# Kernel optimization log

Hardware: AMD Instinct MI355X
Metric: run time of the kernel (lower is better)

## Reference

```python
import jax, jax.numpy as jnp
import numpy as np

N = 50000
E = 800000
IN_CH = 128
HID = 128
HEADS = 8
OUT_CH = 40
NEG_SLOPE = 0.2
BN_EPS = 1e-5


def gat_conv(x, src, dst, W, a_src, a_dst, bias, heads, ch, concat):
    # x: [N, F_in]; W: [heads*ch, F_in]; a_src/a_dst: [heads, ch]; bias: [heads*ch] or [ch]
    n = x.shape[0]
    h = (x @ W.T).reshape(n, heads, ch)                      # [N, H, C]
    alpha_src = (h * a_src[None]).sum(-1)                    # [N, H]
    alpha_dst = (h * a_dst[None]).sum(-1)                    # [N, H]
    e = alpha_src[src] + alpha_dst[dst]                      # [E, H]
    e = jax.nn.leaky_relu(e, NEG_SLOPE)
    # segment softmax over incoming edges of each destination node
    emax = jax.ops.segment_max(e, dst, num_segments=n)       # [N, H]
    ee = jnp.exp(e - emax[dst])
    denom = jax.ops.segment_sum(ee, dst, num_segments=n)     # [N, H]
    alpha = ee / (denom[dst] + 1e-16)                        # [E, H]
    msg = h[src] * alpha[:, :, None]                         # [E, H, C]
    out = jax.ops.segment_sum(msg, dst, num_segments=n)      # [N, H, C]
    out = out.reshape(n, heads * ch) if concat else out.mean(axis=1)
    return out + bias


def batch_norm_eval(x, gamma, beta, mean, var):
    return (x - mean) * jax.lax.rsqrt(var + BN_EPS) * gamma + beta


def setup_inputs() -> dict:
    key = jax.random.key(0)
    ks = jax.random.split(key, 16)
    ch = HID // HEADS  # 16
    s = 1.0 / np.sqrt(IN_CH)
    inp = {
        "x": jax.random.normal(ks[0], (N, IN_CH), dtype=jnp.float32),
        "edge_index": jax.random.randint(ks[1], (2, E), 0, N, dtype=jnp.int64),
        # layer 0
        "W0": jax.random.normal(ks[2], (HEADS * ch, IN_CH), jnp.float32) * s,
        "a_src0": jax.random.normal(ks[3], (HEADS, ch), jnp.float32) * 0.1,
        "a_dst0": jax.random.normal(ks[4], (HEADS, ch), jnp.float32) * 0.1,
        "b0": jnp.zeros((HID,), jnp.float32),
        "bn_g0": jnp.ones((HID,), jnp.float32),
        "bn_b0": jnp.zeros((HID,), jnp.float32),
        "bn_m0": jnp.zeros((HID,), jnp.float32),
        "bn_v0": jnp.ones((HID,), jnp.float32),
        # layer 1
        "W1": jax.random.normal(ks[5], (HEADS * ch, HID), jnp.float32) * (1.0 / np.sqrt(HID)),
        "a_src1": jax.random.normal(ks[6], (HEADS, ch), jnp.float32) * 0.1,
        "a_dst1": jax.random.normal(ks[7], (HEADS, ch), jnp.float32) * 0.1,
        "b1": jnp.zeros((HID,), jnp.float32),
        "bn_g1": jnp.ones((HID,), jnp.float32),
        "bn_b1": jnp.zeros((HID,), jnp.float32),
        "bn_m1": jnp.zeros((HID,), jnp.float32),
        "bn_v1": jnp.ones((HID,), jnp.float32),
        # output layer (heads=1, concat=False)
        "W2": jax.random.normal(ks[8], (OUT_CH, HID), jnp.float32) * (1.0 / np.sqrt(HID)),
        "a_src2": jax.random.normal(ks[9], (1, OUT_CH), jnp.float32) * 0.1,
        "a_dst2": jax.random.normal(ks[10], (1, OUT_CH), jnp.float32) * 0.1,
        "b2": jnp.zeros((OUT_CH,), jnp.float32),
    }
    return inp


def reference(x, edge_index, W0, a_src0, a_dst0, b0, bn_g0, bn_b0, bn_m0, bn_v0,
              W1, a_src1, a_dst1, b1, bn_g1, bn_b1, bn_m1, bn_v1,
              W2, a_src2, a_dst2, b2):
    n = x.shape[0]
    # PyG GATConv adds self-loops by default
    loops = jnp.arange(n, dtype=edge_index.dtype)
    src = jnp.concatenate([edge_index[0], loops])
    dst = jnp.concatenate([edge_index[1], loops])
    ch = HID // HEADS

    h = gat_conv(x, src, dst, W0, a_src0, a_dst0, b0, HEADS, ch, True)
    h = batch_norm_eval(h, bn_g0, bn_b0, bn_m0, bn_v0)
    h = jax.nn.elu(h)
    # dropout: eval mode (identity)

    h = gat_conv(h, src, dst, W1, a_src1, a_dst1, b1, HEADS, ch, True)
    h = batch_norm_eval(h, bn_g1, bn_b1, bn_m1, bn_v1)
    h = jax.nn.elu(h)

    out = gat_conv(h, src, dst, W2, a_src2, a_dst2, b2, 1, OUT_CH, False)
    return out
```

## Files before the change

### kernel.cpp

```cpp
#include <hip/hip_runtime.h>
#include <hip/hip_fp16.h>
#include <math.h>

constexpr float NEG_SLOPE = 0.2f;
constexpr float BN_EPS_C = 1e-5f;

using half8 = __attribute__((ext_vector_type(8))) _Float16;
using half4 = __attribute__((ext_vector_type(4))) _Float16;
using f32x4 = __attribute__((ext_vector_type(4))) float;


__global__ __launch_bounds__(256)
void hist_cvt_kernel(const int* __restrict__ ei, int* __restrict__ bucket_count,
                     int E, int N, int NEB,
                     const float* __restrict__ W0, const float* __restrict__ W1,
                     const float* __restrict__ W2,
                     __half* __restrict__ W0h, __half* __restrict__ W1h,
                     __half* __restrict__ W2h) {
    int t = threadIdx.x;
    if ((int)blockIdx.x >= NEB) {
        int i = ((int)blockIdx.x - NEB) * 256 + t;
        if (i < 16384) {
            W0h[i] = __float2half(W0[i]);
            W1h[i] = __float2half(W1[i]);
        }
        if (i < 6144) W2h[i] = __float2half(i < 5120 ? W2[i] : 0.f);
        return;
    }
    __shared__ int h[256];
    h[t] = 0;
    __syncthreads();
    int base = blockIdx.x * 8192;
    int ET = E + N;
#pragma unroll
    for (int q = 0; q < 32; ++q) {
        int i = base + q * 256 + t;
        if (i < ET) {
            int d = (i < E) ? ei[E + i] : (i - E);
            atomicAdd(&h[d >> 8], 1);
        }
    }
    __syncthreads();
    if (h[t] > 0) atomicAdd(&bucket_count[t], h[t]);
}

__global__ __launch_bounds__(256)
void bucket_scan_kernel(const int* __restrict__ bucket_count, int* __restrict__ bucket_ptr,
                        int* __restrict__ gcursor, int* __restrict__ row_ptr,
                        int N, int ET) {
    __shared__ int s[256];
    int t = threadIdx.x;
    int c = bucket_count[t];
    s[t] = c;
    __syncthreads();
    for (int off = 1; off < 256; off <<= 1) {
        int v = (t >= off) ? s[t - off] : 0;
        __syncthreads();
        s[t] += v;
        __syncthreads();
    }
    int excl = s[t] - c;
    bucket_ptr[t] = excl;
    gcursor[t] = excl;
    if (t == 255) {
        bucket_ptr[256] = s[255];
        row_ptr[N] = ET;
    }
}

__global__ __launch_bounds__(256)
void bucket_bin_kernel(const int* __restrict__ ei, int* __restrict__ gcursor,
                       unsigned* __restrict__ tmp, int E, int N) {
    __shared__ unsigned bins[8192];
    __shared__ int lcount[256];
    __shared__ int lofs[256];
    __shared__ int lbase[256];
    __shared__ int lcur[256];
    int t = threadIdx.x;
    lcount[t] = 0;
    __syncthreads();
    int base = blockIdx.x * 8192;
    int ET = E + N;
    unsigned pr[32];
#pragma unroll
    for (int q = 0; q < 32; ++q) {
        int i = base + q * 256 + t;
        pr[q] = 0xFFFFFFFFu;
        if (i < ET) {
            int s, d;
            if (i < E) { s = ei[i]; d = ei[E + i]; }
            else       { s = i - E; d = s; }
            pr[q] = ((unsigned)d << 16) | (unsigned)s;
            atomicAdd(&lcount[d >> 8], 1);
        }
    }
    __syncthreads();
    {
        int c = lcount[t];
        lofs[t] = c;
        __syncthreads();
        for (int off = 1; off < 256; off <<= 1) {
            int v = (t >= off) ? lofs[t - off] : 0;
            __syncthreads();
            lofs[t] += v;
            __syncthreads();
        }
        int excl = lofs[t] - c;
        __syncthreads();
        lofs[t] = excl;
        lcur[t] = excl;
        if (c > 0) lbase[t] = atomicAdd(&gcursor[t], c);
    }
    __syncthreads();
#pragma unroll
    for (int q = 0; q < 32; ++q) {
        if (pr[q] != 0xFFFFFFFFu) {
            int b = pr[q] >> 24;
            int p = atomicAdd(&lcur[b], 1);
            bins[p] = pr[q];
        }
    }
    __syncthreads();
    int total = min(8192, ET - base);
    for (int p = t; p < total; p += 256) {
        unsigned e = bins[p];
        int b = e >> 24;
        tmp[lbase[b] + (p - lofs[b])] = e;
    }
}

__global__ __launch_bounds__(256)
void fine_scatter_kernel(const unsigned* __restrict__ tmp, const int* __restrict__ bucket_ptr,
                         int* __restrict__ row_ptr, int* __restrict__ srcs, int N) {
    __shared__ int hist[256];
    __shared__ int scanb[256];
    __shared__ int cur[256];
    int b = blockIdx.x, t = threadIdx.x;
    int base = bucket_ptr[b];
    int cnt = bucket_ptr[b + 1] - base;
    int n0 = b << 8;
    hist[t] = 0;
    __syncthreads();
    for (int p = t; p < cnt; p += 256)
        atomicAdd(&hist[(int)(tmp[base + p] >> 16) - n0], 1);
    __syncthreads();
    int c = hist[t];
    scanb[t] = c;
    __syncthreads();
    for (int off = 1; off < 256; off <<= 1) {
        int v = (t >= off) ? scanb[t - off] : 0;
        __syncthreads();
        scanb[t] += v;
        __syncthreads();
    }
    int excl = scanb[t] - c;
    cur[t] = excl;
    if (n0 + t < N) row_ptr[n0 + t] = base + excl;
    __syncthreads();
    for (int p = t; p < cnt; p += 256) {
        unsigned e = tmp[base + p];
        int pos = atomicAdd(&cur[(int)(e >> 16) - n0], 1);
        srcs[base + pos] = (int)(e & 0xFFFFu);
    }
}


template<bool AHALF>
__global__ __launch_bounds__(512)
void gemm128_mfma_kernel(const void* __restrict__ Xv, const __half* __restrict__ W16,
                         const float* __restrict__ a_src, const float* __restrict__ a_dst,
                         __half* __restrict__ hp, float* __restrict__ asrc,
                         float* __restrict__ adst, int N) {
    __shared__ _Float16 Bs[128][136];
    const int t = threadIdx.x;
    const int n0 = blockIdx.x * 128;

#pragma unroll
    for (int i = 0; i < 4; ++i) {
        int lin = t + i * 512;
        int n = lin >> 4;
        int m = lin & 15;
        *reinterpret_cast<uint4*>(&Bs[n][8 * m]) =
            *reinterpret_cast<const uint4*>(&W16[(size_t)n * 128 + 8 * m]);
    }
    __syncthreads();

    const int l  = t & 63;
    const int w  = t >> 6;
    const int lr = l & 15;
    const int lg = l >> 4;
    const int rowA = n0 + 16 * w + lr;
    const bool rokA = rowA < N;

    f32x4 acc[8];
#pragma unroll
    for (int tt = 0; tt < 8; ++tt) acc[tt] = (f32x4){0.f, 0.f, 0.f, 0.f};

#pragma unroll
    for (int ks = 0; ks < 4; ++ks) {
        half8 a;
        if (rokA) {
            if constexpr (AHALF) {
                const __half* X = (const __half*)Xv;
                a = *reinterpret_cast<const half8*>(&X[(size_t)rowA * 128 + 8 * lg + 32 * ks]);
            } else {
                const float* X = (const float*)Xv;
                const float* p = &X[(size_t)rowA * 128 + 8 * lg + 32 * ks];
                float4 v0 = *reinterpret_cast<const float4*>(p);
                float4 v1 = *reinterpret_cast<const float4*>(p + 4);
                a[0] = (_Float16)v0.x; a[1] = (_Float16)v0.y;
                a[2] = (_Float16)v0.z; a[3] = (_Float16)v0.w;
                a[4] = (_Float16)v1.x; a[5] = (_Float16)v1.y;
                a[6] = (_Float16)v1.z; a[7] = (_Float16)v1.w;
            }
        } else {
#pragma unroll
            for (int q = 0; q < 8; ++q) a[q] = (_Float16)0.f;
        }
#pragma unroll
        for (int tt = 0; tt < 8; ++tt) {
            half8 b = *reinterpret_cast<const half8*>(&Bs[16 * tt + lr][8 * lg + 32 * ks]);
            acc[tt] = __builtin_amdgcn_mfma_f32_16x16x32_f16(a, b, acc[tt], 0, 0, 0);
        }
    }

    float av[8], bv[8];
#pragma unroll
    for (int tt = 0; tt < 8; ++tt) {
        av[tt] = a_src[16 * tt + lr];
        bv[tt] = a_dst[16 * tt + lr];
    }
#pragma unroll
    for (int reg = 0; reg < 4; ++reg) {
        int gr = n0 + 16 * w + 4 * lg + reg;
        bool ok = gr < N;
        if (ok) {
#pragma unroll
            for (int tt = 0; tt < 8; ++tt)
                hp[(size_t)gr * 128 + 16 * tt + lr] = __float2half(acc[tt][reg]);
        }
#pragma unroll
        for (int tt = 0; tt < 8; ++tt) {
            float p = acc[tt][reg] * av[tt];
            float q = acc[tt][reg] * bv[tt];
#pragma unroll
            for (int off = 1; off < 16; off <<= 1) {
                p += __shfl_xor(p, off, 16);
                q += __shfl_xor(q, off, 16);
            }
            if (ok && lr == tt) {
                asrc[(size_t)gr * 8 + tt] = p;
                adst[(size_t)gr * 8 + tt] = q;
            }
        }
    }
}


__global__ __launch_bounds__(256)
void gemm40_mfma_kernel(const __half* __restrict__ X, const __half* __restrict__ W16,
                        const float* __restrict__ a_src, const float* __restrict__ a_dst,
                        __half* __restrict__ hp, float* __restrict__ asrc,
                        float* __restrict__ adst, int N) {
    __shared__ _Float16 Bs[48][136];
    const int t = threadIdx.x;
    const int n0 = blockIdx.x * 64;

#pragma unroll
    for (int i = 0; i < 3; ++i) {
        int lin = t + i * 256;
        if (lin < 768) {
            int n = lin >> 4;
            int m = lin & 15;
            *reinterpret_cast<uint4*>(&Bs[n][8 * m]) =
                *reinterpret_cast<const uint4*>(&W16[(size_t)n * 128 + 8 * m]);
        }
    }
    __syncthreads();

    const int l  = t & 63;
    const int w  = t >> 6;
    const int lr = l & 15;
    const int lg = l >> 4;
    const int rowA = n0 + 16 * w + lr;
    const bool rokA = rowA < N;

    f32x4 acc[3];
#pragma unroll
    for (int tt = 0; tt < 3; ++tt) acc[tt] = (f32x4){0.f, 0.f, 0.f, 0.f};

#pragma unroll
    for (int ks = 0; ks < 4; ++ks) {
        half8 a;
        if (rokA) {
            a = *reinterpret_cast<const half8*>(&X[(size_t)rowA * 128 + 8 * lg + 32 * ks]);
        } else {
#pragma unroll
            for (int q = 0; q < 8; ++q) a[q] = (_Float16)0.f;
        }
#pragma unroll
        for (int tt = 0; tt < 3; ++tt) {
            half8 b = *reinterpret_cast<const half8*>(&Bs[16 * tt + lr][8 * lg + 32 * ks]);
            acc[tt] = __builtin_amdgcn_mfma_f32_16x16x32_f16(a, b, acc[tt], 0, 0, 0);
        }
    }

    float av[3], bv[3];
#pragma unroll
    for (int tt = 0; tt < 3; ++tt) {
        int j = 16 * tt + lr;
        av[tt] = (j < 40) ? a_src[j] : 0.f;
        bv[tt] = (j < 40) ? a_dst[j] : 0.f;
    }
#pragma unroll
    for (int reg = 0; reg < 4; ++reg) {
        int gr = n0 + 16 * w + 4 * lg + reg;
        bool ok = gr < N;
        float p = 0.f, q = 0.f;
#pragma unroll
        for (int tt = 0; tt < 3; ++tt) {
            int j = 16 * tt + lr;
            if (ok && j < 40) hp[(size_t)gr * 40 + j] = __float2half(acc[tt][reg]);
            p += acc[tt][reg] * av[tt];
            q += acc[tt][reg] * bv[tt];
        }
#pragma unroll
        for (int off = 1; off < 16; off <<= 1) {
            p += __shfl_xor(p, off, 16);
            q += __shfl_xor(q, off, 16);
        }
        if (ok && lr == 0) {
            asrc[gr] = p;
            adst[gr] = q;
        }
    }
}


__global__ __launch_bounds__(256)
void message128_kernel(const __half* __restrict__ hh, const int* __restrict__ row_ptr,
                       const int* __restrict__ srcs,
                       const float* __restrict__ asrc, const float* __restrict__ adst,
                       const float* __restrict__ bias,
                       const float* __restrict__ bn_g, const float* __restrict__ bn_b,
                       const float* __restrict__ bn_m, const float* __restrict__ bn_v,
                       __half* __restrict__ out16, int N) {
    int node = blockIdx.x * 8 + (threadIdx.x >> 5);
    if (node >= N) return;
    int tc = threadIdx.x & 31;
    int half_id = tc >> 4;
    int cl = tc & 15;
    int hd = cl >> 1;
    int beg = row_ptr[node], end = row_ptr[node + 1];
    float ad = adst[(size_t)node * 8 + hd];
    float ssum = 0.f;
    float acc[8];
#pragma unroll
    for (int q = 0; q < 8; ++q) acc[q] = 0.f;

    int j = beg;
    for (; j + 4 <= end; j += 4) {
        int sA = srcs[j + half_id];
        int sB = srcs[j + 2 + half_id];
        half8 vA = *reinterpret_cast<const half8*>(&hh[(size_t)sA * 128 + 8 * cl]);
        half8 vB = *reinterpret_cast<const half8*>(&hh[(size_t)sB * 128 + 8 * cl]);
        float eA = asrc[(size_t)sA * 8 + hd] + ad;
        float eB = asrc[(size_t)sB * 8 + hd] + ad;
        eA = (eA > 0.f) ? eA : NEG_SLOPE * eA;
        eB = (eB > 0.f) ? eB : NEG_SLOPE * eB;
        float wA = __expf(eA);
        float wB = __expf(eB);
        ssum += wA + wB;
#pragma unroll
        for (int q = 0; q < 8; ++q) {
            acc[q] = fmaf((float)vA[q], wA, acc[q]);
            acc[q] = fmaf((float)vB[q], wB, acc[q]);
        }
    }
    for (; j + 2 <= end; j += 2) {
        int s = srcs[j + half_id];
        half8 v = *reinterpret_cast<const half8*>(&hh[(size_t)s * 128 + 8 * cl]);
        float e = asrc[(size_t)s * 8 + hd] + ad;
        e = (e > 0.f) ? e : NEG_SLOPE * e;
        float wgt = __expf(e);
        ssum += wgt;
#pragma unroll
        for (int q = 0; q < 8; ++q) acc[q] = fmaf((float)v[q], wgt, acc[q]);
    }
    if (j < end && half_id == 0) {
        int s = srcs[j];
        half8 v = *reinterpret_cast<const half8*>(&hh[(size_t)s * 128 + 8 * cl]);
        float e = asrc[(size_t)s * 8 + hd] + ad;
        e = (e > 0.f) ? e : NEG_SLOPE * e;
        float wgt = __expf(e);
        ssum += wgt;
#pragma unroll
        for (int q = 0; q < 8; ++q) acc[q] = fmaf((float)v[q], wgt, acc[q]);
    }
    ssum += __shfl_xor(ssum, 16);
#pragma unroll
    for (int q = 0; q < 8; ++q) acc[q] += __shfl_xor(acc[q], 16);

    if (half_id == 0) {
        float inv = 1.0f / (ssum + 1e-16f);
        int c = cl * 8;
        float r[8];
#pragma unroll
        for (int pp = 0; pp < 2; ++pp) {
            int cc = c + 4 * pp;
            float4 bi = *reinterpret_cast<const float4*>(&bias[cc]);
            float4 g  = *reinterpret_cast<const float4*>(&bn_g[cc]);
            float4 bb = *reinterpret_cast<const float4*>(&bn_b[cc]);
            float4 mm = *reinterpret_cast<const float4*>(&bn_m[cc]);
            float4 vv = *reinterpret_cast<const float4*>(&bn_v[cc]);
            r[4 * pp + 0] = (acc[4 * pp + 0] * inv + bi.x - mm.x) * rsqrtf(vv.x + BN_EPS_C) * g.x + bb.x;
            r[4 * pp + 1] = (acc[4 * pp + 1] * inv + bi.y - mm.y) * rsqrtf(vv.y + BN_EPS_C) * g.y + bb.y;
            r[4 * pp + 2] = (acc[4 * pp + 2] * inv + bi.z - mm.z) * rsqrtf(vv.z + BN_EPS_C) * g.z + bb.z;
            r[4 * pp + 3] = (acc[4 * pp + 3] * inv + bi.w - mm.w) * rsqrtf(vv.w + BN_EPS_C) * g.w + bb.w;
        }
        half8 o;
#pragma unroll
        for (int q = 0; q < 8; ++q) {
            float rv = (r[q] > 0.f) ? r[q] : expm1f(r[q]);
            o[q] = (_Float16)rv;
        }
        *reinterpret_cast<half8*>(&out16[(size_t)node * 128 + c]) = o;
    }
}


__global__ __launch_bounds__(256)
void message40_kernel(const __half* __restrict__ hh2, const int* __restrict__ row_ptr,
                      const int* __restrict__ srcs,
                      const float* __restrict__ asrc, const float* __restrict__ adst,
                      const float* __restrict__ b2, float* __restrict__ out, int N) {
    int node = blockIdx.x * 16 + (threadIdx.x >> 4);
    if (node >= N) return;
    int tc = threadIdx.x & 15;
    int beg = row_ptr[node], end = row_ptr[node + 1];
    float ad = adst[node];
    float ssum = 0.f;
    float acc[4] = {0.f, 0.f, 0.f, 0.f};
    int j = beg;
    for (; j + 2 <= end; j += 2) {
        int s0 = srcs[j];
        int s1 = srcs[j + 1];
        half4 v0 = (half4){0, 0, 0, 0}, v1 = (half4){0, 0, 0, 0};
        if (tc < 10) {
            v0 = *reinterpret_cast<const half4*>(&hh2[(size_t)s0 * 40 + 4 * tc]);
            v1 = *reinterpret_cast<const half4*>(&hh2[(size_t)s1 * 40 + 4 * tc]);
        }
        float e0 = asrc[s0] + ad;
        float e1 = asrc[s1] + ad;
        e0 = (e0 > 0.f) ? e0 : NEG_SLOPE * e0;
        e1 = (e1 > 0.f) ? e1 : NEG_SLOPE * e1;
        float w0 = __expf(e0);
        float w1 = __expf(e1);
        ssum += w0 + w1;
#pragma unroll
        for (int q = 0; q < 4; ++q) {
            acc[q] = fmaf((float)v0[q], w0, acc[q]);
            acc[q] = fmaf((float)v1[q], w1, acc[q]);
        }
    }
    if (j < end) {
        int s0 = srcs[j];
        half4 v0 = (half4){0, 0, 0, 0};
        if (tc < 10) v0 = *reinterpret_cast<const half4*>(&hh2[(size_t)s0 * 40 + 4 * tc]);
        float e0 = asrc[s0] + ad;
        e0 = (e0 > 0.f) ? e0 : NEG_SLOPE * e0;
        float w0 = __expf(e0);
        ssum += w0;
#pragma unroll
        for (int q = 0; q < 4; ++q) acc[q] = fmaf((float)v0[q], w0, acc[q]);
    }
    if (tc < 10) {
        float inv = 1.0f / (ssum + 1e-16f);
        int c = tc * 4;
        float4 bi = *reinterpret_cast<const float4*>(&b2[c]);
        *reinterpret_cast<float4*>(&out[(size_t)node * 40 + c]) =
            make_float4(acc[0] * inv + bi.x, acc[1] * inv + bi.y,
                        acc[2] * inv + bi.z, acc[3] * inv + bi.w);
    }
}


static inline char* align256(char* p) {
    return (char*)(((uintptr_t)p + 255) & ~(uintptr_t)255);
}

extern "C" void kernel_launch(void* const* d_in, const int* in_sizes, int n_in,
                              void* d_out, int out_size, void* d_ws, size_t ws_size,
                              hipStream_t stream) {
    const float* x   = (const float*)d_in[0];
    const int*   ei  = (const int*)d_in[1];
    const float* W0  = (const float*)d_in[2];
    const float* as0 = (const float*)d_in[3];
    const float* ad0 = (const float*)d_in[4];
    const float* b0  = (const float*)d_in[5];
    const float* g0  = (const float*)d_in[6];
    const float* bb0 = (const float*)d_in[7];
    const float* m0  = (const float*)d_in[8];
    const float* v0  = (const float*)d_in[9];
    const float* W1  = (const float*)d_in[10];
    const float* as1 = (const float*)d_in[11];
    const float* ad1 = (const float*)d_in[12];
    const float* b1  = (const float*)d_in[13];
    const float* g1  = (const float*)d_in[14];
    const float* bb1 = (const float*)d_in[15];
    const float* m1  = (const float*)d_in[16];
    const float* v1  = (const float*)d_in[17];
    const float* W2  = (const float*)d_in[18];
    const float* as2 = (const float*)d_in[19];
    const float* ad2 = (const float*)d_in[20];
    const float* b2  = (const float*)d_in[21];

    const int N  = in_sizes[0] / 128;
    const int E  = in_sizes[1] / 2;
    const int ET = E + N;
    const int NBUK = (N + 255) >> 8;
    const int NEB  = (ET + 8191) / 8192;

    char* wsp = (char*)d_ws;
    int* bucket_count = (int*)wsp;  wsp = align256(wsp + 256 * 4);
    int* bucket_ptr   = (int*)wsp;  wsp = align256(wsp + 257 * 4);
    int* gcursor      = (int*)wsp;  wsp = align256(wsp + 256 * 4);
    int* row_ptr      = (int*)wsp;  wsp = align256(wsp + (size_t)(N + 1) * 4);
    unsigned* tmp     = (unsigned*)wsp; wsp = align256(wsp + (size_t)ET * 4);
    int* srcs         = (int*)wsp;  wsp = align256(wsp + (size_t)ET * 4);
    __half* hh        = (__half*)wsp; wsp = align256(wsp + (size_t)N * 128 * 2);
    __half* h2        = (__half*)wsp; wsp = align256(wsp + (size_t)N * 40 * 2);
    __half* feat      = (__half*)wsp; wsp = align256(wsp + (size_t)N * 128 * 2);
    float* asr        = (float*)wsp;  wsp = align256(wsp + (size_t)N * 8 * 4);
    float* adt        = (float*)wsp;  wsp = align256(wsp + (size_t)N * 8 * 4);
    __half* W0h       = (__half*)wsp; wsp = align256(wsp + 16384 * 2);
    __half* W1h       = (__half*)wsp; wsp = align256(wsp + 16384 * 2);
    __half* W2h       = (__half*)wsp; wsp = align256(wsp + 6144 * 2);

    hipMemsetAsync(bucket_count, 0, 256 * 4, stream);
    hist_cvt_kernel<<<NEB + 64, 256, 0, stream>>>(ei, bucket_count, E, N, NEB,
                                                  W0, W1, W2, W0h, W1h, W2h);
    bucket_scan_kernel<<<1, 256, 0, stream>>>(bucket_count, bucket_ptr, gcursor, row_ptr, N, ET);
    bucket_bin_kernel<<<NEB, 256, 0, stream>>>(ei, gcursor, tmp, E, N);
    fine_scatter_kernel<<<NBUK, 256, 0, stream>>>(tmp, bucket_ptr, row_ptr, srcs, N);

    const int g128 = (N + 127) / 128;
    const int g64  = (N + 63) / 64;

    gemm128_mfma_kernel<false><<<g128, 512, 0, stream>>>(x, W0h, as0, ad0, hh, asr, adt, N);
    message128_kernel<<<(N + 7) / 8, 256, 0, stream>>>(hh, row_ptr, srcs, asr, adt,
                                                       b0, g0, bb0, m0, v0, feat, N);
    gemm128_mfma_kernel<true><<<g128, 512, 0, stream>>>(feat, W1h, as1, ad1, hh, asr, adt, N);
    message128_kernel<<<(N + 7) / 8, 256, 0, stream>>>(hh, row_ptr, srcs, asr, adt,
                                                       b1, g1, bb1, m1, v1, feat, N);
    gemm40_mfma_kernel<<<g64, 256, 0, stream>>>(feat, W2h, as2, ad2, h2, asr, adt, N);
    message40_kernel<<<(N + 15) / 16, 256, 0, stream>>>(h2, row_ptr, srcs,
                                                        asr, adt, b2, (float*)d_out, N);
}
```

Before: 213.4 us.

## Store hidden features head-sliced and split message passing per head slice

Hidden features and attention logits move from node-major to head-slice-major storage ([8][N][16] and [8][N]). The GEMMs write and read this layout, and the message kernel now gives each block one head slice for four nodes. A wavefront handles 16 edges at once with 4 lanes per edge and reduces across lanes with shuffles. The goal is to keep each slice's gather working set small enough for L2 and to parallelise over edges, at the cost of 8x more blocks and per-slice rereads of srcs and row_ptr.

```diff
diff --git a/kernel.cpp b/kernel.cpp
--- a/kernel.cpp
+++ b/kernel.cpp
@@ -202,7 +202,11 @@
         if (rokA) {
             if constexpr (AHALF) {
                 const __half* X = (const __half*)Xv;
-                a = *reinterpret_cast<const half8*>(&X[(size_t)rowA * 128 + 8 * lg + 32 * ks]);
+                int ch = 8 * lg + 32 * ks;
+                int sl = ch >> 4;
+                int off = ch & 15;
+                a = *reinterpret_cast<const half8*>(
+                    &X[(size_t)sl * N * 16 + (size_t)rowA * 16 + off]);
             } else {
                 const float* X = (const float*)Xv;
                 const float* p = &X[(size_t)rowA * 128 + 8 * lg + 32 * ks];
@@ -237,7 +241,7 @@
         if (ok) {
 #pragma unroll
             for (int tt = 0; tt < 8; ++tt)
-                hp[(size_t)gr * 128 + 16 * tt + lr] = __float2half(acc[tt][reg]);
+                hp[(size_t)tt * N * 16 + (size_t)gr * 16 + lr] = __float2half(acc[tt][reg]);
         }
 #pragma unroll
         for (int tt = 0; tt < 8; ++tt) {
@@ -249,8 +253,8 @@
                 q += __shfl_xor(q, off, 16);
             }
             if (ok && lr == tt) {
-                asrc[(size_t)gr * 8 + tt] = p;
-                adst[(size_t)gr * 8 + tt] = q;
+                asrc[(size_t)tt * N + gr] = p;
+                adst[(size_t)tt * N + gr] = q;
             }
         }
     }
@@ -293,7 +297,11 @@
     for (int ks = 0; ks < 4; ++ks) {
         half8 a;
         if (rokA) {
-            a = *reinterpret_cast<const half8*>(&X[(size_t)rowA * 128 + 8 * lg + 32 * ks]);
+            int ch = 8 * lg + 32 * ks;
+            int sl = ch >> 4;
+            int off = ch & 15;
+            a = *reinterpret_cast<const half8*>(
+                &X[(size_t)sl * N * 16 + (size_t)rowA * 16 + off]);
         } else {
 #pragma unroll
             for (int q = 0; q < 8; ++q) a[q] = (_Float16)0.f;
@@ -338,93 +346,68 @@
 
 
 __global__ __launch_bounds__(256)
-void message128_kernel(const __half* __restrict__ hh, const int* __restrict__ row_ptr,
+void message128_kernel(const __half* __restrict__ hhs, const int* __restrict__ row_ptr,
                        const int* __restrict__ srcs,
-                       const float* __restrict__ asrc, const float* __restrict__ adst,
+                       const float* __restrict__ asrc_s, const float* __restrict__ adst_s,
                        const float* __restrict__ bias,
                        const float* __restrict__ bn_g, const float* __restrict__ bn_b,
                        const float* __restrict__ bn_m, const float* __restrict__ bn_v,
-                       __half* __restrict__ out16, int N) {
-    int node = blockIdx.x * 8 + (threadIdx.x >> 5);
+                       __half* __restrict__ feat_s, int N) {
+    const int slice = blockIdx.x & 7;
+    const int node = (blockIdx.x >> 3) * 4 + (threadIdx.x >> 6);
     if (node >= N) return;
-    int tc = threadIdx.x & 31;
-    int half_id = tc >> 4;
-    int cl = tc & 15;
-    int hd = cl >> 1;
-    int beg = row_ptr[node], end = row_ptr[node + 1];
-    float ad = adst[(size_t)node * 8 + hd];
+    const int l = threadIdx.x & 63;
+    const int e = l >> 2;
+    const int q = l & 3;
+    const int beg = row_ptr[node], end = row_ptr[node + 1];
+    const __half* hsl = hhs + (size_t)slice * N * 16;
+    const float*  asl = asrc_s + (size_t)slice * N;
+    const float ad = adst_s[(size_t)slice * N + node];
+
     float ssum = 0.f;
-    float acc[8];
-#pragma unroll
-    for (int q = 0; q < 8; ++q) acc[q] = 0.f;
-
-    int j = beg;
-    for (; j + 4 <= end; j += 4) {
-        int sA = srcs[j + half_id];
-        int sB = srcs[j + 2 + half_id];
-        half8 vA = *reinterpret_cast<const half8*>(&hh[(size_t)sA * 128 + 8 * cl]);
-        half8 vB = *reinterpret_cast<const half8*>(&hh[(size_t)sB * 128 + 8 * cl]);
-        float eA = asrc[(size_t)sA * 8 + hd] + ad;
-        float eB = asrc[(size_t)sB * 8 + hd] + ad;
-        eA = (eA > 0.f) ? eA : NEG_SLOPE * eA;
-        eB = (eB > 0.f) ? eB : NEG_SLOPE * eB;
-        float wA = __expf(eA);
-        float wB = __expf(eB);
-        ssum += wA + wB;
-#pragma unroll
-        for (int q = 0; q < 8; ++q) {
-            acc[q] = fmaf((float)vA[q], wA, acc[q]);
-            acc[q] = fmaf((float)vB[q], wB, acc[q]);
-        }
-    }
-    for (; j + 2 <= end; j += 2) {
-        int s = srcs[j + half_id];
-        half8 v = *reinterpret_cast<const half8*>(&hh[(size_t)s * 128 + 8 * cl]);
-        float e = asrc[(size_t)s * 8 + hd] + ad;
-        e = (e > 0.f) ? e : NEG_SLOPE * e;
-        float wgt = __expf(e);
-        ssum += wgt;
-#pragma unroll
-        for (int q = 0; q < 8; ++q) acc[q] = fmaf((float)v[q], wgt, acc[q]);
-    }
-    if (j < end && half_id == 0) {
-        int s = srcs[j];
-        half8 v = *reinterpret_cast<const half8*>(&hh[(size_t)s * 128 + 8 * cl]);
-        float e = asrc[(size_t)s * 8 + hd] + ad;
-        e = (e > 0.f) ? e : NEG_SLOPE * e;
-        float wgt = __expf(e);
-        ssum += wgt;
-#pragma unroll
-        for (int q = 0; q < 8; ++q) acc[q] = fmaf((float)v[q], wgt, acc[q]);
-    }
-    ssum += __shfl_xor(ssum, 16);
-#pragma unroll
-    for (int q = 0; q < 8; ++q) acc[q] += __shfl_xor(acc[q], 16);
-
-    if (half_id == 0) {
+    float acc[4] = {0.f, 0.f, 0.f, 0.f};
+    for (int j = beg; j < end; j += 16) {
+        int idx = j + e;
+        float w = 0.f;
+        half4 v = (half4){0, 0, 0, 0};
+        if (idx < end) {
+            int s = srcs[idx];
+            v = *reinterpret_cast<const half4*>(&hsl[(size_t)s * 16 + 4 * q]);
+            float ea = asl[s] + ad;
+            ea = (ea > 0.f) ? ea : NEG_SLOPE * ea;
+            w = __expf(ea);
+        }
+        ssum += w;
+#pragma unroll
+        for (int k = 0; k < 4; ++k) acc[k] = fmaf((float)v[k], w, acc[k]);
+    }
+#pragma unroll
+    for (int off = 4; off < 64; off <<= 1) {
+        ssum += __shfl_xor(ssum, off);
+#pragma unroll
+        for (int k = 0; k < 4; ++k) acc[k] += __shfl_xor(acc[k], off);
+    }
+
+    if (e == 0) {
         float inv = 1.0f / (ssum + 1e-16f);
-        int c = cl * 8;
-        float r[8];
-#pragma unroll
-        for (int pp = 0; pp < 2; ++pp) {
-            int cc = c + 4 * pp;
-            float4 bi = *reinterpret_cast<const float4*>(&bias[cc]);
-            float4 g  = *reinterpret_cast<const float4*>(&bn_g[cc]);
-            float4 bb = *reinterpret_cast<const float4*>(&bn_b[cc]);
-            float4 mm = *reinterpret_cast<const float4*>(&bn_m[cc]);
-            float4 vv = *reinterpret_cast<const float4*>(&bn_v[cc]);
-            r[4 * pp + 0] = (acc[4 * pp + 0] * inv + bi.x - mm.x) * rsqrtf(vv.x + BN_EPS_C) * g.x + bb.x;
-            r[4 * pp + 1] = (acc[4 * pp + 1] * inv + bi.y - mm.y) * rsqrtf(vv.y + BN_EPS_C) * g.y + bb.y;
-            r[4 * pp + 2] = (acc[4 * pp + 2] * inv + bi.z - mm.z) * rsqrtf(vv.z + BN_EPS_C) * g.z + bb.z;
-            r[4 * pp + 3] = (acc[4 * pp + 3] * inv + bi.w - mm.w) * rsqrtf(vv.w + BN_EPS_C) * g.w + bb.w;
-        }
-        half8 o;
-#pragma unroll
-        for (int q = 0; q < 8; ++q) {
-            float rv = (r[q] > 0.f) ? r[q] : expm1f(r[q]);
-            o[q] = (_Float16)rv;
-        }
-        *reinterpret_cast<half8*>(&out16[(size_t)node * 128 + c]) = o;
+        int c = slice * 16 + 4 * q;
+        float4 bi = *reinterpret_cast<const float4*>(&bias[c]);
+        float4 g  = *reinterpret_cast<const float4*>(&bn_g[c]);
+        float4 bb = *reinterpret_cast<const float4*>(&bn_b[c]);
+        float4 mm = *reinterpret_cast<const float4*>(&bn_m[c]);
+        float4 vv = *reinterpret_cast<const float4*>(&bn_v[c]);
+        float r0 = (acc[0] * inv + bi.x - mm.x) * rsqrtf(vv.x + BN_EPS_C) * g.x + bb.x;
+        float r1 = (acc[1] * inv + bi.y - mm.y) * rsqrtf(vv.y + BN_EPS_C) * g.y + bb.y;
+        float r2 = (acc[2] * inv + bi.z - mm.z) * rsqrtf(vv.z + BN_EPS_C) * g.z + bb.z;
+        float r3 = (acc[3] * inv + bi.w - mm.w) * rsqrtf(vv.w + BN_EPS_C) * g.w + bb.w;
+        r0 = (r0 > 0.f) ? r0 : expm1f(r0);
+        r1 = (r1 > 0.f) ? r1 : expm1f(r1);
+        r2 = (r2 > 0.f) ? r2 : expm1f(r2);
+        r3 = (r3 > 0.f) ? r3 : expm1f(r3);
+        half4 o;
+        o[0] = (_Float16)r0; o[1] = (_Float16)r1;
+        o[2] = (_Float16)r2; o[3] = (_Float16)r3;
+        *reinterpret_cast<half4*>(&feat_s[(size_t)slice * N * 16 + (size_t)node * 16 + 4 * q]) = o;
     }
 }
 
@@ -546,13 +529,14 @@
 
     const int g128 = (N + 127) / 128;
     const int g64  = (N + 63) / 64;
+    const int gmsg = ((N + 3) / 4) * 8;
 
     gemm128_mfma_kernel<false><<<g128, 512, 0, stream>>>(x, W0h, as0, ad0, hh, asr, adt, N);
-    message128_kernel<<<(N + 7) / 8, 256, 0, stream>>>(hh, row_ptr, srcs, asr, adt,
-                                                       b0, g0, bb0, m0, v0, feat, N);
+    message128_kernel<<<gmsg, 256, 0, stream>>>(hh, row_ptr, srcs, asr, adt,
+                                                b0, g0, bb0, m0, v0, feat, N);
     gemm128_mfma_kernel<true><<<g128, 512, 0, stream>>>(feat, W1h, as1, ad1, hh, asr, adt, N);
-    message128_kernel<<<(N + 7) / 8, 256, 0, stream>>>(hh, row_ptr, srcs, asr, adt,
-                                                       b1, g1, bb1, m1, v1, feat, N);
+    message128_kernel<<<gmsg, 256, 0, stream>>>(hh, row_ptr, srcs, asr, adt,
+                                                b1, g1, bb1, m1, v1, feat, N);
     gemm40_mfma_kernel<<<g64, 256, 0, stream>>>(feat, W2h, as2, ad2, h2, asr, adt, N);
     message40_kernel<<<(N + 15) / 16, 256, 0, stream>>>(h2, row_ptr, srcs,
                                                         asr, adt, b2, (float*)d_out, N);
```

Result: slower. 425.5 us (+99.4%).

## Split GAT layers into edge-weight precompute and head-sliced aggregation

Applied to the files above, without the earlier changes.

Adds separate kernels that compute per-edge attention weights (stored as fp16, head-major) and per-node inverse softmax denominators. The 128-wide features move to a head-sliced layout ([8][N][16]), and the aggregation kernel now runs one block slice per head, so each gathered row fits in a small contiguous region. The aim is to take exp and leaky-relu work out of the gather loop and to improve cache locality per head slice. The cost is extra kernel launches, writing and reading an ET*8 fp16 weight array, fp16 rounding of the weights, and edge indices being re-read by every head slice.

```diff
diff --git a/kernel.cpp b/kernel.cpp
--- a/kernel.cpp
+++ b/kernel.cpp
@@ -202,7 +202,11 @@
         if (rokA) {
             if constexpr (AHALF) {
                 const __half* X = (const __half*)Xv;
-                a = *reinterpret_cast<const half8*>(&X[(size_t)rowA * 128 + 8 * lg + 32 * ks]);
+                int ch = 8 * lg + 32 * ks;
+                int sl = ch >> 4;
+                int off = ch & 15;
+                a = *reinterpret_cast<const half8*>(
+                    &X[(size_t)sl * N * 16 + (size_t)rowA * 16 + off]);
             } else {
                 const float* X = (const float*)Xv;
                 const float* p = &X[(size_t)rowA * 128 + 8 * lg + 32 * ks];
@@ -237,7 +241,7 @@
         if (ok) {
 #pragma unroll
             for (int tt = 0; tt < 8; ++tt)
-                hp[(size_t)gr * 128 + 16 * tt + lr] = __float2half(acc[tt][reg]);
+                hp[(size_t)tt * N * 16 + (size_t)gr * 16 + lr] = __float2half(acc[tt][reg]);
         }
 #pragma unroll
         for (int tt = 0; tt < 8; ++tt) {
@@ -293,7 +297,11 @@
     for (int ks = 0; ks < 4; ++ks) {
         half8 a;
         if (rokA) {
-            a = *reinterpret_cast<const half8*>(&X[(size_t)rowA * 128 + 8 * lg + 32 * ks]);
+            int ch = 8 * lg + 32 * ks;
+            int sl = ch >> 4;
+            int off = ch & 15;
+            a = *reinterpret_cast<const half8*>(
+                &X[(size_t)sl * N * 16 + (size_t)rowA * 16 + off]);
         } else {
 #pragma unroll
             for (int q = 0; q < 8; ++q) a[q] = (_Float16)0.f;
@@ -338,125 +346,138 @@
 
 
 __global__ __launch_bounds__(256)
-void message128_kernel(const __half* __restrict__ hh, const int* __restrict__ row_ptr,
+void weight8_kernel(const int* __restrict__ row_ptr, const int* __restrict__ srcs,
+                    const float* __restrict__ as8, const float* __restrict__ ad8,
+                    __half* __restrict__ ew, float* __restrict__ inv, int N, int ET) {
+    int gid = blockIdx.x * 256 + threadIdx.x;
+    int node = gid >> 3;
+    int h = gid & 7;
+    if (node >= N) return;
+    int beg = row_ptr[node], end = row_ptr[node + 1];
+    float ad = ad8[(size_t)node * 8 + h];
+    float sum = 0.f;
+    for (int j = beg; j < end; ++j) {
+        int s = srcs[j];
+        float e = as8[(size_t)s * 8 + h] + ad;
+        e = (e > 0.f) ? e : NEG_SLOPE * e;
+        float w = __expf(e);
+        sum += w;
+        ew[(size_t)h * ET + j] = __float2half(w);
+    }
+    inv[(size_t)h * N + node] = 1.0f / (sum + 1e-16f);
+}
+
+
+__global__ __launch_bounds__(256)
+void weight1_kernel(const int* __restrict__ row_ptr, const int* __restrict__ srcs,
+                    const float* __restrict__ as, const float* __restrict__ ad,
+                    __half* __restrict__ ew, float* __restrict__ inv, int N) {
+    int node = blockIdx.x * 256 + threadIdx.x;
+    if (node >= N) return;
+    int beg = row_ptr[node], end = row_ptr[node + 1];
+    float a = ad[node];
+    float sum = 0.f;
+    for (int j = beg; j < end; ++j) {
+        int s = srcs[j];
+        float e = as[s] + a;
+        e = (e > 0.f) ? e : NEG_SLOPE * e;
+        float w = __expf(e);
+        sum += w;
+        ew[j] = __float2half(w);
+    }
+    inv[node] = 1.0f / (sum + 1e-16f);
+}
+
+
+__global__ __launch_bounds__(256)
+void message128_kernel(const __half* __restrict__ hhs, const int* __restrict__ row_ptr,
                        const int* __restrict__ srcs,
-                       const float* __restrict__ asrc, const float* __restrict__ adst,
+                       const __half* __restrict__ ew, const float* __restrict__ inv,
                        const float* __restrict__ bias,
                        const float* __restrict__ bn_g, const float* __restrict__ bn_b,
                        const float* __restrict__ bn_m, const float* __restrict__ bn_v,
-                       __half* __restrict__ out16, int N) {
-    int node = blockIdx.x * 8 + (threadIdx.x >> 5);
+                       __half* __restrict__ feat_s, int N, int ET) {
+    const int slice = blockIdx.x & 7;
+    const int node = (blockIdx.x >> 3) * 128 + (threadIdx.x >> 1);
     if (node >= N) return;
-    int tc = threadIdx.x & 31;
-    int half_id = tc >> 4;
-    int cl = tc & 15;
-    int hd = cl >> 1;
-    int beg = row_ptr[node], end = row_ptr[node + 1];
-    float ad = adst[(size_t)node * 8 + hd];
-    float ssum = 0.f;
+    const int hl = threadIdx.x & 1;
+    const int beg = row_ptr[node], end = row_ptr[node + 1];
+    const __half* hsl = hhs + (size_t)slice * N * 16 + 8 * hl;
+    const __half* ews = ew + (size_t)slice * ET;
+
     float acc[8];
 #pragma unroll
-    for (int q = 0; q < 8; ++q) acc[q] = 0.f;
+    for (int k = 0; k < 8; ++k) acc[k] = 0.f;
 
     int j = beg;
-    for (; j + 4 <= end; j += 4) {
-        int sA = srcs[j + half_id];
-        int sB = srcs[j + 2 + half_id];
-        half8 vA = *reinterpret_cast<const half8*>(&hh[(size_t)sA * 128 + 8 * cl]);
-        half8 vB = *reinterpret_cast<const half8*>(&hh[(size_t)sB * 128 + 8 * cl]);
-        float eA = asrc[(size_t)sA * 8 + hd] + ad;
-        float eB = asrc[(size_t)sB * 8 + hd] + ad;
-        eA = (eA > 0.f) ? eA : NEG_SLOPE * eA;
-        eB = (eB > 0.f) ? eB : NEG_SLOPE * eB;
-        float wA = __expf(eA);
-        float wB = __expf(eB);
-        ssum += wA + wB;
-#pragma unroll
-        for (int q = 0; q < 8; ++q) {
-            acc[q] = fmaf((float)vA[q], wA, acc[q]);
-            acc[q] = fmaf((float)vB[q], wB, acc[q]);
-        }
-    }
     for (; j + 2 <= end; j += 2) {
-        int s = srcs[j + half_id];
-        half8 v = *reinterpret_cast<const half8*>(&hh[(size_t)s * 128 + 8 * cl]);
-        float e = asrc[(size_t)s * 8 + hd] + ad;
-        e = (e > 0.f) ? e : NEG_SLOPE * e;
-        float wgt = __expf(e);
-        ssum += wgt;
-#pragma unroll
-        for (int q = 0; q < 8; ++q) acc[q] = fmaf((float)v[q], wgt, acc[q]);
-    }
-    if (j < end && half_id == 0) {
-        int s = srcs[j];
-        half8 v = *reinterpret_cast<const half8*>(&hh[(size_t)s * 128 + 8 * cl]);
-        float e = asrc[(size_t)s * 8 + hd] + ad;
-        e = (e > 0.f) ? e : NEG_SLOPE * e;
-        float wgt = __expf(e);
-        ssum += wgt;
-#pragma unroll
-        for (int q = 0; q < 8; ++q) acc[q] = fmaf((float)v[q], wgt, acc[q]);
-    }
-    ssum += __shfl_xor(ssum, 16);
-#pragma unroll
-    for (int q = 0; q < 8; ++q) acc[q] += __shfl_xor(acc[q], 16);
-
-    if (half_id == 0) {
-        float inv = 1.0f / (ssum + 1e-16f);
-        int c = cl * 8;
-        float r[8];
-#pragma unroll
-        for (int pp = 0; pp < 2; ++pp) {
-            int cc = c + 4 * pp;
-            float4 bi = *reinterpret_cast<const float4*>(&bias[cc]);
-            float4 g  = *reinterpret_cast<const float4*>(&bn_g[cc]);
-            float4 bb = *reinterpret_cast<const float4*>(&bn_b[cc]);
-            float4 mm = *reinterpret_cast<const float4*>(&bn_m[cc]);
-            float4 vv = *reinterpret_cast<const float4*>(&bn_v[cc]);
-            r[4 * pp + 0] = (acc[4 * pp + 0] * inv + bi.x - mm.x) * rsqrtf(vv.x + BN_EPS_C) * g.x + bb.x;
-            r[4 * pp + 1] = (acc[4 * pp + 1] * inv + bi.y - mm.y) * rsqrtf(vv.y + BN_EPS_C) * g.y + bb.y;
-            r[4 * pp + 2] = (acc[4 * pp + 2] * inv + bi.z - mm.z) * rsqrtf(vv.z + BN_EPS_C) * g.z + bb.z;
-            r[4 * pp + 3] = (acc[4 * pp + 3] * inv + bi.w - mm.w) * rsqrtf(vv.w + BN_EPS_C) * g.w + bb.w;
-        }
-        half8 o;
-#pragma unroll
-        for (int q = 0; q < 8; ++q) {
-            float rv = (r[q] > 0.f) ? r[q] : expm1f(r[q]);
-            o[q] = (_Float16)rv;
-        }
-        *reinterpret_cast<half8*>(&out16[(size_t)node * 128 + c]) = o;
-    }
+        int s0 = srcs[j];
+        int s1 = srcs[j + 1];
+        float w0 = __half2float(ews[j]);
+        float w1 = __half2float(ews[j + 1]);
+        half8 v0 = *reinterpret_cast<const half8*>(&hsl[(size_t)s0 * 16]);
+        half8 v1 = *reinterpret_cast<const half8*>(&hsl[(size_t)s1 * 16]);
+#pragma unroll
+        for (int k = 0; k < 8; ++k) {
+            acc[k] = fmaf((float)v0[k], w0, acc[k]);
+            acc[k] = fmaf((float)v1[k], w1, acc[k]);
+        }
+    }
+    if (j < end) {
+        int s0 = srcs[j];
+        float w0 = __half2float(ews[j]);
+        half8 v0 = *reinterpret_cast<const half8*>(&hsl[(size_t)s0 * 16]);
+#pragma unroll
+        for (int k = 0; k < 8; ++k) acc[k] = fmaf((float)v0[k], w0, acc[k]);
+    }
+
+    float iv = inv[(size_t)slice * N + node];
+    int c = slice * 16 + 8 * hl;
+    float r[8];
+#pragma unroll
+    for (int pp = 0; pp < 2; ++pp) {
+        int cc = c + 4 * pp;
+        float4 bi = *reinterpret_cast<const float4*>(&bias[cc]);
+        float4 g  = *reinterpret_cast<const float4*>(&bn_g[cc]);
+        float4 bb = *reinterpret_cast<const float4*>(&bn_b[cc]);
+        float4 mm = *reinterpret_cast<const float4*>(&bn_m[cc]);
+        float4 vv = *reinterpret_cast<const float4*>(&bn_v[cc]);
+        r[4 * pp + 0] = (acc[4 * pp + 0] * iv + bi.x - mm.x) * rsqrtf(vv.x + BN_EPS_C) * g.x + bb.x;
+        r[4 * pp + 1] = (acc[4 * pp + 1] * iv + bi.y - mm.y) * rsqrtf(vv.y + BN_EPS_C) * g.y + bb.y;
+        r[4 * pp + 2] = (acc[4 * pp + 2] * iv + bi.z - mm.z) * rsqrtf(vv.z + BN_EPS_C) * g.z + bb.z;
+        r[4 * pp + 3] = (acc[4 * pp + 3] * iv + bi.w - mm.w) * rsqrtf(vv.w + BN_EPS_C) * g.w + bb.w;
+    }
+    half8 o;
+#pragma unroll
+    for (int k = 0; k < 8; ++k) {
+        float rv = (r[k] > 0.f) ? r[k] : expm1f(r[k]);
+        o[k] = (_Float16)rv;
+    }
+    *reinterpret_cast<half8*>(&feat_s[(size_t)slice * N * 16 + (size_t)node * 16 + 8 * hl]) = o;
 }
 
 
 __global__ __launch_bounds__(256)
 void message40_kernel(const __half* __restrict__ hh2, const int* __restrict__ row_ptr,
                       const int* __restrict__ srcs,
-                      const float* __restrict__ asrc, const float* __restrict__ adst,
+                      const __half* __restrict__ ew, const float* __restrict__ inv,
                       const float* __restrict__ b2, float* __restrict__ out, int N) {
     int node = blockIdx.x * 16 + (threadIdx.x >> 4);
     if (node >= N) return;
     int tc = threadIdx.x & 15;
     int beg = row_ptr[node], end = row_ptr[node + 1];
-    float ad = adst[node];
-    float ssum = 0.f;
     float acc[4] = {0.f, 0.f, 0.f, 0.f};
     int j = beg;
     for (; j + 2 <= end; j += 2) {
         int s0 = srcs[j];
         int s1 = srcs[j + 1];
+        float w0 = __half2float(ew[j]);
+        float w1 = __half2float(ew[j + 1]);
         half4 v0 = (half4){0, 0, 0, 0}, v1 = (half4){0, 0, 0, 0};
         if (tc < 10) {
             v0 = *reinterpret_cast<const half4*>(&hh2[(size_t)s0 * 40 + 4 * tc]);
             v1 = *reinterpret_cast<const half4*>(&hh2[(size_t)s1 * 40 + 4 * tc]);
         }
-        float e0 = asrc[s0] + ad;
-        float e1 = asrc[s1] + ad;
-        e0 = (e0 > 0.f) ? e0 : NEG_SLOPE * e0;
-        e1 = (e1 > 0.f) ? e1 : NEG_SLOPE * e1;
-        float w0 = __expf(e0);
-        float w1 = __expf(e1);
-        ssum += w0 + w1;
 #pragma unroll
         for (int q = 0; q < 4; ++q) {
             acc[q] = fmaf((float)v0[q], w0, acc[q]);
@@ -465,22 +486,19 @@
     }
     if (j < end) {
         int s0 = srcs[j];
+        float w0 = __half2float(ew[j]);
         half4 v0 = (half4){0, 0, 0, 0};
         if (tc < 10) v0 = *reinterpret_cast<const half4*>(&hh2[(size_t)s0 * 40 + 4 * tc]);
-        float e0 = asrc[s0] + ad;
-        e0 = (e0 > 0.f) ? e0 : NEG_SLOPE * e0;
-        float w0 = __expf(e0);
-        ssum += w0;
 #pragma unroll
         for (int q = 0; q < 4; ++q) acc[q] = fmaf((float)v0[q], w0, acc[q]);
     }
     if (tc < 10) {
-        float inv = 1.0f / (ssum + 1e-16f);
+        float iv = inv[node];
         int c = tc * 4;
         float4 bi = *reinterpret_cast<const float4*>(&b2[c]);
         *reinterpret_cast<float4*>(&out[(size_t)node * 40 + c]) =
-            make_float4(acc[0] * inv + bi.x, acc[1] * inv + bi.y,
-                        acc[2] * inv + bi.z, acc[3] * inv + bi.w);
+            make_float4(acc[0] * iv + bi.x, acc[1] * iv + bi.y,
+                        acc[2] * iv + bi.z, acc[3] * iv + bi.w);
     }
 }
 
@@ -533,6 +551,8 @@
     __half* feat      = (__half*)wsp; wsp = align256(wsp + (size_t)N * 128 * 2);
     float* asr        = (float*)wsp;  wsp = align256(wsp + (size_t)N * 8 * 4);
     float* adt        = (float*)wsp;  wsp = align256(wsp + (size_t)N * 8 * 4);
+    __half* ew        = (__half*)wsp; wsp = align256(wsp + (size_t)ET * 8 * 2);
+    float* inv        = (float*)wsp;  wsp = align256(wsp + (size_t)N * 8 * 4);
     __half* W0h       = (__half*)wsp; wsp = align256(wsp + 16384 * 2);
     __half* W1h       = (__half*)wsp; wsp = align256(wsp + 16384 * 2);
     __half* W2h       = (__half*)wsp; wsp = align256(wsp + 6144 * 2);
@@ -546,14 +566,20 @@
 
     const int g128 = (N + 127) / 128;
     const int g64  = (N + 63) / 64;
+    const int gw8  = (N * 8 + 255) / 256;
+    const int gw1  = (N + 255) / 256;
+    const int gmsg = ((N + 127) / 128) * 8;
 
     gemm128_mfma_kernel<false><<<g128, 512, 0, stream>>>(x, W0h, as0, ad0, hh, asr, adt, N);
-    message128_kernel<<<(N + 7) / 8, 256, 0, stream>>>(hh, row_ptr, srcs, asr, adt,
-                                                       b0, g0, bb0, m0, v0, feat, N);
+    weight8_kernel<<<gw8, 256, 0, stream>>>(row_ptr, srcs, asr, adt, ew, inv, N, ET);
+    message128_kernel<<<gmsg, 256, 0, stream>>>(hh, row_ptr, srcs, ew, inv,
+                                                b0, g0, bb0, m0, v0, feat, N, ET);
     gemm128_mfma_kernel<true><<<g128, 512, 0, stream>>>(feat, W1h, as1, ad1, hh, asr, adt, N);
-    message128_kernel<<<(N + 7) / 8, 256, 0, stream>>>(hh, row_ptr, srcs, asr, adt,
-                                                       b1, g1, bb1, m1, v1, feat, N);
+    weight8_kernel<<<gw8, 256, 0, stream>>>(row_ptr, srcs, asr, adt, ew, inv, N, ET);
+    message128_kernel<<<gmsg, 256, 0, stream>>>(hh, row_ptr, srcs, ew, inv,
+                                                b1, g1, bb1, m1, v1, feat, N, ET);
     gemm40_mfma_kernel<<<g64, 256, 0, stream>>>(feat, W2h, as2, ad2, h2, asr, adt, N);
-    message40_kernel<<<(N + 15) / 16, 256, 0, stream>>>(h2, row_ptr, srcs,
-                                                        asr, adt, b2, (float*)d_out, N);
-}
+    weight1_kernel<<<gw1, 256, 0, stream>>>(row_ptr, srcs, asr, adt, ew, inv, N);
+    message40_kernel<<<(N + 15) / 16, 256, 0, stream>>>(h2, row_ptr, srcs, ew, inv,
+                                                        b2, (float*)d_out, N);
+}
```

Result: slower. 346.7 us (+62.5%).
